# Optimization experiments

Measured on AMD Instinct MI355X. Metric: run time of the kernel, lower is better.

The kernel has to match this reference:

```python
import jax, jax.numpy as jnp
import numpy as np

N_NODES = 100000
N_EDGES = 3200000
N_FEAT = 16
N_GRAPHS = 1024


def setup_inputs() -> dict:
    key = jax.random.key(0)
    ks = jax.random.split(key, 12)
    x = jax.random.normal(ks[0], (N_NODES, N_FEAT), dtype=jnp.float32)
    edge_index = jax.random.randint(ks[1], (2, N_EDGES), 0, N_NODES, dtype=jnp.int32)
    batch = jnp.sort(jax.random.randint(ks[2], (N_NODES,), 0, N_GRAPHS, dtype=jnp.int32))
    def lin(k, fan_in, fan_out):
        s = 1.0 / np.sqrt(fan_in)
        return jax.random.uniform(k, (fan_in, fan_out), jnp.float32, -s, s)
    W1 = lin(ks[3], N_FEAT, 64); b1 = jnp.zeros((64,), jnp.float32)
    W2 = lin(ks[4], 64, 32);     b2 = jnp.zeros((32,), jnp.float32)
    fc1_W = lin(ks[5], 32, 16);  fc1_b = jnp.zeros((16,), jnp.float32)
    fc2_W = lin(ks[6], 16, 1);   fc2_b = jnp.zeros((1,), jnp.float32)
    return {"x": x, "edge_index": edge_index, "batch": batch,
            "W1": W1, "b1": b1, "W2": W2, "b2": b2,
            "fc1_W": fc1_W, "fc1_b": fc1_b, "fc2_W": fc2_W, "fc2_b": fc2_b}


def _gcn_conv(h, W, b, src, dst, norm, n_nodes):
    # h: [N, Fin] -> [N, Fout]; symmetric-normalized scatter-add (PyG GCNConv)
    h = h @ W
    msg = h[src] * norm[:, None]            # edge-wise gather + scale
    out = jax.ops.segment_sum(msg, dst, num_segments=n_nodes)
    return out + b


def reference(x, edge_index, batch, W1, b1, W2, b2, fc1_W, fc1_b, fc2_W, fc2_b):
    n_nodes = x.shape[0]
    # add self-loops
    loops = jnp.arange(n_nodes, dtype=edge_index.dtype)
    src = jnp.concatenate([edge_index[0], loops])
    dst = jnp.concatenate([edge_index[1], loops])
    deg = jax.ops.segment_sum(jnp.ones_like(dst, dtype=x.dtype), dst, num_segments=n_nodes)
    dinv = jnp.where(deg > 0, jax.lax.rsqrt(deg), 0.0)
    norm = dinv[src] * dinv[dst]

    h = jax.nn.relu(_gcn_conv(x, W1, b1, src, dst, norm, n_nodes))
    # dropout p=0.2 is identity at inference
    h = jax.nn.relu(_gcn_conv(h, W2, b2, src, dst, norm, n_nodes))

    # global mean pool over graphs
    sums = jax.ops.segment_sum(h, batch, num_segments=N_GRAPHS)
    cnts = jax.ops.segment_sum(jnp.ones((n_nodes,), h.dtype), batch, num_segments=N_GRAPHS)
    g = sums / jnp.maximum(cnts, 1.0)[:, None]

    g = jax.nn.relu(g @ fc1_W + fc1_b)
    # dropout p=0.5 is identity at inference
    out = g @ fc2_W + fc2_b
    return jax.nn.sigmoid(out)  # [N_GRAPHS, 1]
```

## Files before the change

### kernel.cpp

```cpp
#include <hip/hip_runtime.h>
#include <math.h>

#define NNODES  100000
#define NEDGES  3200000
#define NGRAPHS 1024
#define BNODES  196
#define NBUCK   ((NNODES + BNODES - 1) / BNODES)
#define SCAP    12288
#define CHUNK   4096
#define NCHUNKS ((NEDGES + CHUNK - 1) / CHUNK)

typedef int iv4 __attribute__((ext_vector_type(4)));
typedef float fv2 __attribute__((ext_vector_type(2)));

#if defined(__has_builtin)
#if __has_builtin(__builtin_amdgcn_cvt_pk_f32_fp8) && __has_builtin(__builtin_amdgcn_cvt_pk_fp8_f32)
#define HW_FP8 1
#endif
#endif

__device__ __forceinline__ unsigned bf16pair(float a, float b) {
    unsigned ua = __float_as_uint(a), ub = __float_as_uint(b);
    ua += 0x7fffu + ((ua >> 16) & 1u);
    ub += 0x7fffu + ((ub >> 16) & 1u);
    return (ua >> 16) | (ub & 0xffff0000u);
}
__device__ __forceinline__ float bflo(unsigned u) { return __uint_as_float(u << 16); }
__device__ __forceinline__ float bfhi(unsigned u) { return __uint_as_float(u & 0xffff0000u); }

__device__ __forceinline__ unsigned fp8_of(float v) {
    unsigned s = (__float_as_uint(v) >> 24) & 0x80u;
    float a = fminf(fabsf(v), 448.f);
    unsigned ub = __float_as_uint(a);
    unsigned lsb = (ub >> 20) & 1u;
    ub += 0x0007FFFFu + lsb;
    int em = (int)(ub >> 20) - (120 << 3);
    if (em < 1) return s;
    if (em > 0x7E) em = 0x7E;
    return s | (unsigned)em;
}
__device__ __forceinline__ float fp8_to_f(unsigned b) {
    unsigned em = b & 0x7Fu;
    unsigned s = (b & 0x80u) << 24;
    float f = __uint_as_float(s | ((em + 0x3C0u) << 20));
    return (em >= 8u) ? f : 0.f;
}
__device__ __forceinline__ void fp8x4_to_f(unsigned w, float& f0, float& f1, float& f2, float& f3) {
#ifdef HW_FP8
    fv2 lo = __builtin_amdgcn_cvt_pk_f32_fp8((int)w, false);
    fv2 hi = __builtin_amdgcn_cvt_pk_f32_fp8((int)w, true);
    f0 = lo.x; f1 = lo.y; f2 = hi.x; f3 = hi.y;
#else
    f0 = fp8_to_f(w & 0xFFu);
    f1 = fp8_to_f((w >> 8) & 0xFFu);
    f2 = fp8_to_f((w >> 16) & 0xFFu);
    f3 = fp8_to_f(w >> 24);
#endif
}
__device__ __forceinline__ unsigned fp8x4_pack(float a, float b, float c, float d) {
    a = fminf(fmaxf(a, -448.f), 448.f);
    b = fminf(fmaxf(b, -448.f), 448.f);
    c = fminf(fmaxf(c, -448.f), 448.f);
    d = fminf(fmaxf(d, -448.f), 448.f);
#ifdef HW_FP8
    int w = __builtin_amdgcn_cvt_pk_fp8_f32(a, b, 0, false);
    w = __builtin_amdgcn_cvt_pk_fp8_f32(c, d, w, true);
    return (unsigned)w;
#else
    return fp8_of(a) | (fp8_of(b) << 8) | (fp8_of(c) << 16) | (fp8_of(d) << 24);
#endif
}


__global__ void zero4_kernel(int4* p, int nvec) {
    int i = blockIdx.x * blockDim.x + threadIdx.x;
    if (i < nvec) p[i] = make_int4(0, 0, 0, 0);
}


__global__ void binA_kernel(const int* __restrict__ src, const int* __restrict__ dst,
                            int* __restrict__ bucketCur, int* __restrict__ stage) {
    __shared__ int lcnt[NBUCK + 1];
    __shared__ int boff[NBUCK + 1];
    __shared__ int gbase[NBUCK + 1];
    __shared__ int cur[NBUCK + 1];
    __shared__ int ssum[256];
    __shared__ int packed[CHUNK];
    __shared__ unsigned short bof[CHUNK];
    int tid = threadIdx.x;
    int beg = blockIdx.x * CHUNK;
    int end = beg + CHUNK; if (end > NEDGES) end = NEDGES;
    int cnt = end - beg;

    for (int i = tid; i <= NBUCK; i += 256) lcnt[i] = 0;
    __syncthreads();

    int ent[16];
    int bk[16];
#pragma unroll
    for (int it = 0; it < 4; ++it) {
        int e0 = beg + tid * 4 + it * 1024;
        if (e0 < end) {
            iv4 d4 = __builtin_nontemporal_load((const iv4*)(dst + e0));
            iv4 s4 = __builtin_nontemporal_load((const iv4*)(src + e0));
            int b;
            b = d4.x / BNODES; ent[it*4+0] = s4.x | ((d4.x - b*BNODES) << 17); bk[it*4+0] = b; atomicAdd(&lcnt[b], 1);
            b = d4.y / BNODES; ent[it*4+1] = s4.y | ((d4.y - b*BNODES) << 17); bk[it*4+1] = b; atomicAdd(&lcnt[b], 1);
            b = d4.z / BNODES; ent[it*4+2] = s4.z | ((d4.z - b*BNODES) << 17); bk[it*4+2] = b; atomicAdd(&lcnt[b], 1);
            b = d4.w / BNODES; ent[it*4+3] = s4.w | ((d4.w - b*BNODES) << 17); bk[it*4+3] = b; atomicAdd(&lcnt[b], 1);
        } else {
            bk[it*4+0] = -1; bk[it*4+1] = -1; bk[it*4+2] = -1; bk[it*4+3] = -1;
            ent[it*4+0] = 0; ent[it*4+1] = 0; ent[it*4+2] = 0; ent[it*4+3] = 0;
        }
    }
    __syncthreads();

    int b0 = 2 * tid, b1 = 2 * tid + 1;
    int c0 = lcnt[b0];
    int c1 = (b1 < NBUCK) ? lcnt[b1] : 0;
    int sum = c0 + c1;
    ssum[tid] = sum;
    __syncthreads();
    for (int o = 1; o < 256; o <<= 1) {
        int t = (tid >= o) ? ssum[tid - o] : 0;
        __syncthreads();
        ssum[tid] += t;
        __syncthreads();
    }
    int excl = ssum[tid] - sum;
    boff[b0] = excl; cur[b0] = excl;
    if (b1 < NBUCK) { boff[b1] = excl + c0; cur[b1] = excl + c0; }
    if (c0 > 0) gbase[b0] = atomicAdd(&bucketCur[b0], c0);
    if (b1 < NBUCK && c1 > 0) gbase[b1] = atomicAdd(&bucketCur[b1], c1);
    __syncthreads();

#pragma unroll
    for (int k = 0; k < 16; ++k) {
        int b = bk[k];
        if (b >= 0) {
            int p = atomicAdd(&cur[b], 1);
            packed[p] = ent[k];
            bof[p] = (unsigned short)b;
        }
    }
    __syncthreads();

    for (int i = tid; i < cnt; i += 256) {
        int b = bof[i];
        int addr = b * SCAP + gbase[b] + (i - boff[b]);
        stage[addr] = packed[i];
    }
}


__global__ void scanE_kernel(const int* __restrict__ bucketCur, int* __restrict__ ebase) {
    int lane = threadIdx.x;
    int run = 0;
    for (int base = 0; base < NBUCK; base += 64) {
        int idx = base + lane;
        int own = (idx < NBUCK) ? bucketCur[idx] : 0;
        int v = own;
        for (int o = 1; o < 64; o <<= 1) {
            int t = __shfl_up(v, o, 64);
            if (lane >= o) v += t;
        }
        if (idx < NBUCK) ebase[idx] = run + v - own;
        run += __shfl(v, 63, 64);
    }
}


__global__ void binB_kernel(const int* __restrict__ bucketCur, const int* __restrict__ ebase,
                            const int* __restrict__ stage, const float2* __restrict__ x,
                            int* __restrict__ entries, int* __restrict__ rowptr,
                            int* __restrict__ rowend, float* __restrict__ dinv,
                            unsigned* __restrict__ xs) {
    __shared__ int s[256];
    __shared__ int ncur[256];
    __shared__ float ndinv[256];
    int b = blockIdx.x;
    int cntE = bucketCur[b];
    int eb = ebase[b];
    int nlo = b * BNODES;
    int nn = NNODES - nlo; if (nn > BNODES) nn = BNODES;
    int sb = b * SCAP;
    int tid = threadIdx.x;

    s[tid] = 0;
    __syncthreads();
    for (int e = tid; e < cntE; e += 256) {
        unsigned w = (unsigned)stage[sb + e];
        atomicAdd(&s[w >> 17], 1);
    }
    __syncthreads();
    int v = s[tid];
    for (int o = 1; o < 256; o <<= 1) {
        int t = (tid >= o) ? s[tid - o] : 0;
        __syncthreads();
        s[tid] += t;
        __syncthreads();
    }
    int excl = s[tid] - v;
    ncur[tid] = excl;
    if (tid < nn) {
        rowptr[nlo + tid] = eb + excl;
        rowend[nlo + tid] = eb + excl + v;
        float di = rsqrtf((float)(v + 1));
        dinv[nlo + tid] = di;
        ndinv[tid] = di;
    }
    __syncthreads();
    for (int i = tid; i < nn * 8; i += 256) {
        int node = i >> 3, w = i & 7;
        float2 v2 = x[(size_t)(nlo + node) * 8 + w];
        float di = ndinv[node];
        xs[(nlo + node) * 8 + w] = bf16pair(v2.x * di, v2.y * di);
    }
    for (int e = tid; e < cntE; e += 256) {
        unsigned w = (unsigned)stage[sb + e];
        int dl = w >> 17;
        int slot = atomicAdd(&ncur[dl], 1);
        entries[eb + slot] = (int)(w & 0x1FFFFu);
    }
}


__global__ void gather1_mlp_kernel(const int* __restrict__ entries, const int* __restrict__ rowptr,
                                   const int* __restrict__ rowend, const float* __restrict__ dinv,
                                   const unsigned* __restrict__ xs,
                                   const float* __restrict__ W1, const float* __restrict__ b1,
                                   const float* __restrict__ W2, unsigned* __restrict__ hm2f) {
    __shared__ float w1s[16 * 64];
    __shared__ float w2s[64 * 32];
    __shared__ float bb1[64];
    __shared__ float axs[32][17];
    __shared__ float h1s[32][65];
    int tid = threadIdx.x;
    for (int i = tid; i < 16 * 64; i += 256) w1s[i] = W1[i];
    for (int i = tid; i < 64 * 32; i += 256) w2s[i] = W2[i];
    if (tid < 64) bb1[tid] = b1[tid];

    int t = blockIdx.x * 256 + tid;
    int n = t >> 3, lane = t & 7;
    int nl = tid >> 3;
    int beg = rowptr[n], end = rowend[n];
    unsigned self = xs[n * 8 + lane];
    float a0 = bflo(self), a1 = bfhi(self);
    for (int base = beg; base < end; base += 8) {
        int m = end - base; if (m > 8) m = 8;
        int s = (lane < m) ? __builtin_nontemporal_load(entries + base + lane) : 0;
        if (m == 8) {
#pragma unroll
            for (int j = 0; j < 8; ++j) {
                unsigned v = xs[__shfl(s, j, 8) * 8 + lane];
                a0 += bflo(v); a1 += bfhi(v);
            }
        } else {
            for (int j = 0; j < m; ++j) {
                unsigned v = xs[__shfl(s, j, 8) * 8 + lane];
                a0 += bflo(v); a1 += bfhi(v);
            }
        }
    }
    float di = dinv[n];
    axs[nl][lane * 2]     = a0 * di;
    axs[nl][lane * 2 + 1] = a1 * di;
    __syncthreads();

    {
        int j0 = lane * 8;
        float h[8];
#pragma unroll
        for (int jj = 0; jj < 8; ++jj) h[jj] = bb1[j0 + jj];
#pragma unroll
        for (int k = 0; k < 16; ++k) {
            float a = axs[nl][k];
            const float* wr = w1s + k * 64 + j0;
#pragma unroll
            for (int jj = 0; jj < 8; ++jj) h[jj] += a * wr[jj];
        }
#pragma unroll
        for (int jj = 0; jj < 8; ++jj) h1s[nl][j0 + jj] = fmaxf(h[jj], 0.f);
    }
    __syncthreads();

    {
        int j0 = lane * 4;
        float c[4] = {0.f, 0.f, 0.f, 0.f};
#pragma unroll
        for (int k = 0; k < 64; ++k) {
            float hv = h1s[nl][k];
            const float* wr = w2s + k * 32 + j0;
#pragma unroll
            for (int jj = 0; jj < 4; ++jj) c[jj] += hv * wr[jj];
        }
        float sc = di * 64.f;
        hm2f[n * 8 + lane] = fp8x4_pack(c[0] * sc, c[1] * sc, c[2] * sc, c[3] * sc);
    }
}


__global__ void gather2_pool_kernel(const int* __restrict__ entries, const int* __restrict__ rowptr,
                                    const int* __restrict__ rowend, const float* __restrict__ dinv,
                                    const unsigned* __restrict__ hm2f, const float4* __restrict__ b2,
                                    const int* __restrict__ batch,
                                    float* __restrict__ psum, float* __restrict__ pcnt) {
    __shared__ float lps[8][32];
    __shared__ float lpc[8];
    int tid = threadIdx.x;
    ((float*)lps)[tid] = 0.f;
    if (tid < 8) lpc[tid] = 0.f;

    int t = blockIdx.x * 256 + tid;
    int n = t >> 3, lane = t & 7;
    int g0 = batch[(blockIdx.x * 256) >> 3];
    int beg = rowptr[n], end = rowend[n];
    unsigned self = hm2f[n * 8 + lane];
    float a0, a1, a2, a3;
    fp8x4_to_f(self, a0, a1, a2, a3);
    __syncthreads();

    for (int base = beg; base < end; base += 8) {
        int m = end - base; if (m > 8) m = 8;
        int s = (lane < m) ? __builtin_nontemporal_load(entries + base + lane) : 0;
        if (m == 8) {
#pragma unroll
            for (int j = 0; j < 8; ++j) {
                unsigned v = hm2f[__shfl(s, j, 8) * 8 + lane];
                float f0, f1, f2, f3;
                fp8x4_to_f(v, f0, f1, f2, f3);
                a0 += f0; a1 += f1; a2 += f2; a3 += f3;
            }
        } else {
            for (int j = 0; j < m; ++j) {
                unsigned v = hm2f[__shfl(s, j, 8) * 8 + lane];
                float f0, f1, f2, f3;
                fp8x4_to_f(v, f0, f1, f2, f3);
                a0 += f0; a1 += f1; a2 += f2; a3 += f3;
            }
        }
    }
    float sc = dinv[n] * (1.0f / 64.f);
    float4 bb = b2[lane];
    float v0 = fmaxf(a0 * sc + bb.x, 0.f);
    float v1 = fmaxf(a1 * sc + bb.y, 0.f);
    float v2 = fmaxf(a2 * sc + bb.z, 0.f);
    float v3 = fmaxf(a3 * sc + bb.w, 0.f);
    int g = batch[n];
    int gr = g - g0;
    if (gr < 8) {
        float* pg = &lps[gr][lane * 4];
        atomicAdd(pg + 0, v0);
        atomicAdd(pg + 1, v1);
        atomicAdd(pg + 2, v2);
        atomicAdd(pg + 3, v3);
        if (lane == 0) atomicAdd(&lpc[gr], 1.0f);
    } else {
        float* pg = psum + g * 32 + lane * 4;
        atomicAdd(pg + 0, v0);
        atomicAdd(pg + 1, v1);
        atomicAdd(pg + 2, v2);
        atomicAdd(pg + 3, v3);
        if (lane == 0) atomicAdd(&pcnt[g], 1.0f);
    }
    __syncthreads();
    int grf = tid >> 5, f = tid & 31;
    float v = lps[grf][f];
    if (v != 0.f) atomicAdd(&psum[(g0 + grf) * 32 + f], v);
    if (f == 0) {
        float c = lpc[grf];
        if (c != 0.f) atomicAdd(&pcnt[g0 + grf], c);
    }
}


__global__ void head_kernel(const float* __restrict__ psum, const float* __restrict__ pcnt,
                            const float* __restrict__ fc1W, const float* __restrict__ fc1b,
                            const float* __restrict__ fc2W, const float* __restrict__ fc2b,
                            float* __restrict__ out) {
    int g = blockIdx.x * blockDim.x + threadIdx.x;
    if (g >= NGRAPHS) return;
    float inv = 1.0f / fmaxf(pcnt[g], 1.0f);
    float gv[32];
#pragma unroll
    for (int k = 0; k < 32; ++k) gv[k] = psum[g * 32 + k] * inv;
    float o = fc2b[0];
#pragma unroll
    for (int j = 0; j < 16; ++j) {
        float h = fc1b[j];
#pragma unroll
        for (int k = 0; k < 32; ++k) h += gv[k] * fc1W[k * 16 + j];
        h = fmaxf(h, 0.f);
        o += h * fc2W[j];
    }
    out[g] = 1.0f / (1.0f + expf(-o));
}


extern "C" void kernel_launch(void* const* d_in, const int* in_sizes, int n_in,
                              void* d_out, int out_size, void* d_ws, size_t ws_size,
                              hipStream_t stream) {
    const float* x    = (const float*)d_in[0];
    const int*   ei   = (const int*)d_in[1];
    const int*   batch= (const int*)d_in[2];
    const float* W1   = (const float*)d_in[3];
    const float* b1   = (const float*)d_in[4];
    const float* W2   = (const float*)d_in[5];
    const float* b2   = (const float*)d_in[6];
    const float* fc1W = (const float*)d_in[7];
    const float* fc1b = (const float*)d_in[8];
    const float* fc2W = (const float*)d_in[9];
    const float* fc2b = (const float*)d_in[10];
    float* out = (float*)d_out;

    const int* src = ei;
    const int* dst = ei + NEDGES;

    char* wsb = (char*)d_ws;
    int*      bucketCur = (int*)wsb;
    float*    psum      = (float*)(wsb + 2048);
    float*    pcnt      = (float*)(wsb + 133120);
    int*      ebase     = (int*)(wsb + 137216);
    float*    dinv      = (float*)(wsb + 139264);
    int*      rowptr    = (int*)(wsb + 539264);
    int*      rowend    = (int*)(wsb + 939264);
    int*      stage     = (int*)(wsb + 1339392);
    int*      entries   = (int*)(wsb + 26456064);
    unsigned* xs        = (unsigned*)(wsb + 39256064);
    unsigned* hm2f      = (unsigned*)(wsb + 42456064);

    const int B = 256;
    zero4_kernel<<<(8576 + B - 1) / B, B, 0, stream>>>((int4*)wsb, 8576);

    binA_kernel<<<NCHUNKS, B, 0, stream>>>(src, dst, bucketCur, stage);
    scanE_kernel<<<1, 64, 0, stream>>>(bucketCur, ebase);
    binB_kernel<<<NBUCK, B, 0, stream>>>(bucketCur, ebase, stage, (const float2*)x,
                                         entries, rowptr, rowend, dinv, xs);

    gather1_mlp_kernel<<<NNODES * 8 / B, B, 0, stream>>>(entries, rowptr, rowend, dinv, xs,
                                                         W1, b1, W2, hm2f);
    gather2_pool_kernel<<<NNODES * 8 / B, B, 0, stream>>>(entries, rowptr, rowend, dinv,
                                                          hm2f, (const float4*)b2,
                                                          batch, psum, pcnt);
    head_kernel<<<(NGRAPHS + B - 1) / B, B, 0, stream>>>(psum, pcnt, fc1W, fc1b, fc2W, fc2b, out);
}
```

Before: 258.3 us.

## Replace CSR build with per-bucket LDS atomic scatter aggregation

Drops the scan kernel and the second binning pass that built a CSR (rowptr/rowend/entries). Both gather kernels now run one block per destination bucket and stream that bucket's staged (src,dst) words, accumulating messages into a shared-memory accumulator with LDS float atomics. This removes the counting sort and the entries write/read traffic. In exchange it adds heavy LDS atomic contention, fewer blocks (one per 196-node bucket) and a serialized per-chunk MLP loop with extra barriers.

```diff
diff --git a/kernel.cpp b/kernel.cpp
--- a/kernel.cpp
+++ b/kernel.cpp
@@ -153,59 +153,27 @@
 }
 
 
-__global__ void scanE_kernel(const int* __restrict__ bucketCur, int* __restrict__ ebase) {
-    int lane = threadIdx.x;
-    int run = 0;
-    for (int base = 0; base < NBUCK; base += 64) {
-        int idx = base + lane;
-        int own = (idx < NBUCK) ? bucketCur[idx] : 0;
-        int v = own;
-        for (int o = 1; o < 64; o <<= 1) {
-            int t = __shfl_up(v, o, 64);
-            if (lane >= o) v += t;
-        }
-        if (idx < NBUCK) ebase[idx] = run + v - own;
-        run += __shfl(v, 63, 64);
-    }
-}
-
-
-__global__ void binB_kernel(const int* __restrict__ bucketCur, const int* __restrict__ ebase,
-                            const int* __restrict__ stage, const float2* __restrict__ x,
-                            int* __restrict__ entries, int* __restrict__ rowptr,
-                            int* __restrict__ rowend, float* __restrict__ dinv,
-                            unsigned* __restrict__ xs) {
-    __shared__ int s[256];
-    __shared__ int ncur[256];
-    __shared__ float ndinv[256];
+__global__ void binDeg_kernel(const int* __restrict__ bucketCur, const int* __restrict__ stage,
+                              const float2* __restrict__ x, float* __restrict__ dinv,
+                              unsigned* __restrict__ xs) {
+    __shared__ int hist[BNODES];
+    __shared__ float ndinv[BNODES];
     int b = blockIdx.x;
     int cntE = bucketCur[b];
-    int eb = ebase[b];
     int nlo = b * BNODES;
     int nn = NNODES - nlo; if (nn > BNODES) nn = BNODES;
     int sb = b * SCAP;
     int tid = threadIdx.x;
 
-    s[tid] = 0;
+    for (int i = tid; i < BNODES; i += 256) hist[i] = 0;
     __syncthreads();
     for (int e = tid; e < cntE; e += 256) {
         unsigned w = (unsigned)stage[sb + e];
-        atomicAdd(&s[w >> 17], 1);
-    }
-    __syncthreads();
-    int v = s[tid];
-    for (int o = 1; o < 256; o <<= 1) {
-        int t = (tid >= o) ? s[tid - o] : 0;
-        __syncthreads();
-        s[tid] += t;
-        __syncthreads();
-    }
-    int excl = s[tid] - v;
-    ncur[tid] = excl;
+        atomicAdd(&hist[w >> 17], 1);
+    }
+    __syncthreads();
     if (tid < nn) {
-        rowptr[nlo + tid] = eb + excl;
-        rowend[nlo + tid] = eb + excl + v;
-        float di = rsqrtf((float)(v + 1));
+        float di = rsqrtf((float)(hist[tid] + 1));
         dinv[nlo + tid] = di;
         ndinv[tid] = di;
     }
@@ -216,160 +184,164 @@
         float di = ndinv[node];
         xs[(nlo + node) * 8 + w] = bf16pair(v2.x * di, v2.y * di);
     }
-    for (int e = tid; e < cntE; e += 256) {
-        unsigned w = (unsigned)stage[sb + e];
-        int dl = w >> 17;
-        int slot = atomicAdd(&ncur[dl], 1);
-        entries[eb + slot] = (int)(w & 0x1FFFFu);
-    }
-}
-
-
-__global__ void gather1_mlp_kernel(const int* __restrict__ entries, const int* __restrict__ rowptr,
-                                   const int* __restrict__ rowend, const float* __restrict__ dinv,
-                                   const unsigned* __restrict__ xs,
+}
+
+
+__global__ void gather1_mlp_kernel(const int* __restrict__ bucketCur, const int* __restrict__ stage,
+                                   const float* __restrict__ dinv, const unsigned* __restrict__ xs,
                                    const float* __restrict__ W1, const float* __restrict__ b1,
                                    const float* __restrict__ W2, unsigned* __restrict__ hm2f) {
+    __shared__ float accum[BNODES][17];
     __shared__ float w1s[16 * 64];
     __shared__ float w2s[64 * 32];
     __shared__ float bb1[64];
-    __shared__ float axs[32][17];
     __shared__ float h1s[32][65];
     int tid = threadIdx.x;
+    int b = blockIdx.x;
+    int cntE = bucketCur[b];
+    int nlo = b * BNODES;
+    int nn = NNODES - nlo; if (nn > BNODES) nn = BNODES;
+    int sb = b * SCAP;
+    int lane = tid & 7;
+
+    for (int i = tid; i < BNODES * 17; i += 256) ((float*)accum)[i] = 0.f;
     for (int i = tid; i < 16 * 64; i += 256) w1s[i] = W1[i];
     for (int i = tid; i < 64 * 32; i += 256) w2s[i] = W2[i];
     if (tid < 64) bb1[tid] = b1[tid];
-
-    int t = blockIdx.x * 256 + tid;
-    int n = t >> 3, lane = t & 7;
+    __syncthreads();
+
+    for (int e = (tid >> 3); e < cntE; e += 32) {
+        unsigned w = (unsigned)stage[sb + e];
+        int s = (int)(w & 0x1FFFFu);
+        int dl = (int)(w >> 17);
+        unsigned v = xs[s * 8 + lane];
+        atomicAdd(&accum[dl][lane * 2],     bflo(v));
+        atomicAdd(&accum[dl][lane * 2 + 1], bfhi(v));
+    }
+    __syncthreads();
+
     int nl = tid >> 3;
-    int beg = rowptr[n], end = rowend[n];
-    unsigned self = xs[n * 8 + lane];
-    float a0 = bflo(self), a1 = bfhi(self);
-    for (int base = beg; base < end; base += 8) {
-        int m = end - base; if (m > 8) m = 8;
-        int s = (lane < m) ? __builtin_nontemporal_load(entries + base + lane) : 0;
-        if (m == 8) {
-#pragma unroll
-            for (int j = 0; j < 8; ++j) {
-                unsigned v = xs[__shfl(s, j, 8) * 8 + lane];
-                a0 += bflo(v); a1 += bfhi(v);
+    for (int c = 0; c < (BNODES + 31) / 32; ++c) {
+        int node = c * 32 + nl;
+        bool act = node < nn;
+        float di = 0.f;
+        if (act) {
+            di = dinv[nlo + node];
+            unsigned sf = xs[(nlo + node) * 8 + lane];
+            accum[node][lane * 2]     = (accum[node][lane * 2]     + bflo(sf)) * di;
+            accum[node][lane * 2 + 1] = (accum[node][lane * 2 + 1] + bfhi(sf)) * di;
+        }
+        if (act) {
+            int j0 = lane * 8;
+            float h[8];
+#pragma unroll
+            for (int jj = 0; jj < 8; ++jj) h[jj] = bb1[j0 + jj];
+#pragma unroll
+            for (int k = 0; k < 16; ++k) {
+                float a = accum[node][k];
+                const float* wr = w1s + k * 64 + j0;
+#pragma unroll
+                for (int jj = 0; jj < 8; ++jj) h[jj] += a * wr[jj];
             }
-        } else {
-            for (int j = 0; j < m; ++j) {
-                unsigned v = xs[__shfl(s, j, 8) * 8 + lane];
-                a0 += bflo(v); a1 += bfhi(v);
+#pragma unroll
+            for (int jj = 0; jj < 8; ++jj) h1s[nl][j0 + jj] = fmaxf(h[jj], 0.f);
+        }
+        __syncthreads();
+        if (act) {
+            int j0 = lane * 4;
+            float cc[4] = {0.f, 0.f, 0.f, 0.f};
+#pragma unroll
+            for (int k = 0; k < 64; ++k) {
+                float hv = h1s[nl][k];
+                const float* wr = w2s + k * 32 + j0;
+#pragma unroll
+                for (int jj = 0; jj < 4; ++jj) cc[jj] += hv * wr[jj];
             }
-        }
-    }
-    float di = dinv[n];
-    axs[nl][lane * 2]     = a0 * di;
-    axs[nl][lane * 2 + 1] = a1 * di;
-    __syncthreads();
-
-    {
-        int j0 = lane * 8;
-        float h[8];
-#pragma unroll
-        for (int jj = 0; jj < 8; ++jj) h[jj] = bb1[j0 + jj];
-#pragma unroll
-        for (int k = 0; k < 16; ++k) {
-            float a = axs[nl][k];
-            const float* wr = w1s + k * 64 + j0;
-#pragma unroll
-            for (int jj = 0; jj < 8; ++jj) h[jj] += a * wr[jj];
-        }
-#pragma unroll
-        for (int jj = 0; jj < 8; ++jj) h1s[nl][j0 + jj] = fmaxf(h[jj], 0.f);
-    }
-    __syncthreads();
-
-    {
-        int j0 = lane * 4;
-        float c[4] = {0.f, 0.f, 0.f, 0.f};
-#pragma unroll
-        for (int k = 0; k < 64; ++k) {
-            float hv = h1s[nl][k];
-            const float* wr = w2s + k * 32 + j0;
-#pragma unroll
-            for (int jj = 0; jj < 4; ++jj) c[jj] += hv * wr[jj];
-        }
-        float sc = di * 64.f;
-        hm2f[n * 8 + lane] = fp8x4_pack(c[0] * sc, c[1] * sc, c[2] * sc, c[3] * sc);
-    }
-}
-
-
-__global__ void gather2_pool_kernel(const int* __restrict__ entries, const int* __restrict__ rowptr,
-                                    const int* __restrict__ rowend, const float* __restrict__ dinv,
-                                    const unsigned* __restrict__ hm2f, const float4* __restrict__ b2,
-                                    const int* __restrict__ batch,
+            float sc = di * 64.f;
+            hm2f[(nlo + node) * 8 + lane] = fp8x4_pack(cc[0] * sc, cc[1] * sc, cc[2] * sc, cc[3] * sc);
+        }
+        __syncthreads();
+    }
+}
+
+
+__global__ void gather2_pool_kernel(const int* __restrict__ bucketCur, const int* __restrict__ stage,
+                                    const float* __restrict__ dinv, const unsigned* __restrict__ hm2f,
+                                    const float4* __restrict__ b2, const int* __restrict__ batch,
                                     float* __restrict__ psum, float* __restrict__ pcnt) {
+    __shared__ float accum[BNODES][33];
     __shared__ float lps[8][32];
     __shared__ float lpc[8];
     int tid = threadIdx.x;
+    int b = blockIdx.x;
+    int cntE = bucketCur[b];
+    int nlo = b * BNODES;
+    int nn = NNODES - nlo; if (nn > BNODES) nn = BNODES;
+    int sb = b * SCAP;
+    int lane = tid & 7;
+
+    for (int i = tid; i < BNODES * 33; i += 256) ((float*)accum)[i] = 0.f;
     ((float*)lps)[tid] = 0.f;
     if (tid < 8) lpc[tid] = 0.f;
-
-    int t = blockIdx.x * 256 + tid;
-    int n = t >> 3, lane = t & 7;
-    int g0 = batch[(blockIdx.x * 256) >> 3];
-    int beg = rowptr[n], end = rowend[n];
-    unsigned self = hm2f[n * 8 + lane];
-    float a0, a1, a2, a3;
-    fp8x4_to_f(self, a0, a1, a2, a3);
-    __syncthreads();
-
-    for (int base = beg; base < end; base += 8) {
-        int m = end - base; if (m > 8) m = 8;
-        int s = (lane < m) ? __builtin_nontemporal_load(entries + base + lane) : 0;
-        if (m == 8) {
-#pragma unroll
-            for (int j = 0; j < 8; ++j) {
-                unsigned v = hm2f[__shfl(s, j, 8) * 8 + lane];
-                float f0, f1, f2, f3;
-                fp8x4_to_f(v, f0, f1, f2, f3);
-                a0 += f0; a1 += f1; a2 += f2; a3 += f3;
+    int g0 = batch[nlo];
+    __syncthreads();
+
+    for (int e = (tid >> 3); e < cntE; e += 32) {
+        unsigned w = (unsigned)stage[sb + e];
+        int s = (int)(w & 0x1FFFFu);
+        int dl = (int)(w >> 17);
+        unsigned v = hm2f[s * 8 + lane];
+        float f0, f1, f2, f3;
+        fp8x4_to_f(v, f0, f1, f2, f3);
+        float* ar = &accum[dl][lane * 4];
+        atomicAdd(ar + 0, f0);
+        atomicAdd(ar + 1, f1);
+        atomicAdd(ar + 2, f2);
+        atomicAdd(ar + 3, f3);
+    }
+    __syncthreads();
+
+    int nl = tid >> 3;
+    float4 bb = b2[lane];
+    for (int c = 0; c < (BNODES + 31) / 32; ++c) {
+        int node = c * 32 + nl;
+        if (node < nn) {
+            int n = nlo + node;
+            unsigned sf = hm2f[n * 8 + lane];
+            float s0, s1, s2, s3;
+            fp8x4_to_f(sf, s0, s1, s2, s3);
+            float sc = dinv[n] * (1.0f / 64.f);
+            float* ar = &accum[node][lane * 4];
+            float v0 = fmaxf((ar[0] + s0) * sc + bb.x, 0.f);
+            float v1 = fmaxf((ar[1] + s1) * sc + bb.y, 0.f);
+            float v2 = fmaxf((ar[2] + s2) * sc + bb.z, 0.f);
+            float v3 = fmaxf((ar[3] + s3) * sc + bb.w, 0.f);
+            int g = batch[n];
+            int gr = g - g0;
+            if (gr < 8) {
+                float* pg = &lps[gr][lane * 4];
+                atomicAdd(pg + 0, v0);
+                atomicAdd(pg + 1, v1);
+                atomicAdd(pg + 2, v2);
+                atomicAdd(pg + 3, v3);
+                if (lane == 0) atomicAdd(&lpc[gr], 1.0f);
+            } else {
+                float* pg = psum + g * 32 + lane * 4;
+                atomicAdd(pg + 0, v0);
+                atomicAdd(pg + 1, v1);
+                atomicAdd(pg + 2, v2);
+                atomicAdd(pg + 3, v3);
+                if (lane == 0) atomicAdd(&pcnt[g], 1.0f);
             }
-        } else {
-            for (int j = 0; j < m; ++j) {
-                unsigned v = hm2f[__shfl(s, j, 8) * 8 + lane];
-                float f0, f1, f2, f3;
-                fp8x4_to_f(v, f0, f1, f2, f3);
-                a0 += f0; a1 += f1; a2 += f2; a3 += f3;
-            }
-        }
-    }
-    float sc = dinv[n] * (1.0f / 64.f);
-    float4 bb = b2[lane];
-    float v0 = fmaxf(a0 * sc + bb.x, 0.f);
-    float v1 = fmaxf(a1 * sc + bb.y, 0.f);
-    float v2 = fmaxf(a2 * sc + bb.z, 0.f);
-    float v3 = fmaxf(a3 * sc + bb.w, 0.f);
-    int g = batch[n];
-    int gr = g - g0;
-    if (gr < 8) {
-        float* pg = &lps[gr][lane * 4];
-        atomicAdd(pg + 0, v0);
-        atomicAdd(pg + 1, v1);
-        atomicAdd(pg + 2, v2);
-        atomicAdd(pg + 3, v3);
-        if (lane == 0) atomicAdd(&lpc[gr], 1.0f);
-    } else {
-        float* pg = psum + g * 32 + lane * 4;
-        atomicAdd(pg + 0, v0);
-        atomicAdd(pg + 1, v1);
-        atomicAdd(pg + 2, v2);
-        atomicAdd(pg + 3, v3);
-        if (lane == 0) atomicAdd(&pcnt[g], 1.0f);
+        }
     }
     __syncthreads();
     int grf = tid >> 5, f = tid & 31;
     float v = lps[grf][f];
     if (v != 0.f) atomicAdd(&psum[(g0 + grf) * 32 + f], v);
     if (f == 0) {
-        float c = lpc[grf];
-        if (c != 0.f) atomicAdd(&pcnt[g0 + grf], c);
+        float cc = lpc[grf];
+        if (cc != 0.f) atomicAdd(&pcnt[g0 + grf], cc);
     }
 }
 
@@ -420,27 +392,19 @@
     int*      bucketCur = (int*)wsb;
     float*    psum      = (float*)(wsb + 2048);
     float*    pcnt      = (float*)(wsb + 133120);
-    int*      ebase     = (int*)(wsb + 137216);
-    float*    dinv      = (float*)(wsb + 139264);
-    int*      rowptr    = (int*)(wsb + 539264);
-    int*      rowend    = (int*)(wsb + 939264);
-    int*      stage     = (int*)(wsb + 1339392);
-    int*      entries   = (int*)(wsb + 26456064);
-    unsigned* xs        = (unsigned*)(wsb + 39256064);
-    unsigned* hm2f      = (unsigned*)(wsb + 42456064);
+    float*    dinv      = (float*)(wsb + 137216);
+    int*      stage     = (int*)(wsb + 537600);
+    unsigned* xs        = (unsigned*)(wsb + 25654272);
+    unsigned* hm2f      = (unsigned*)(wsb + 28854272);
 
     const int B = 256;
     zero4_kernel<<<(8576 + B - 1) / B, B, 0, stream>>>((int4*)wsb, 8576);
 
     binA_kernel<<<NCHUNKS, B, 0, stream>>>(src, dst, bucketCur, stage);
-    scanE_kernel<<<1, 64, 0, stream>>>(bucketCur, ebase);
-    binB_kernel<<<NBUCK, B, 0, stream>>>(bucketCur, ebase, stage, (const float2*)x,
-                                         entries, rowptr, rowend, dinv, xs);
-
-    gather1_mlp_kernel<<<NNODES * 8 / B, B, 0, stream>>>(entries, rowptr, rowend, dinv, xs,
-                                                         W1, b1, W2, hm2f);
-    gather2_pool_kernel<<<NNODES * 8 / B, B, 0, stream>>>(entries, rowptr, rowend, dinv,
-                                                          hm2f, (const float4*)b2,
-                                                          batch, psum, pcnt);
+    binDeg_kernel<<<NBUCK, B, 0, stream>>>(bucketCur, stage, (const float2*)x, dinv, xs);
+
+    gather1_mlp_kernel<<<NBUCK, B, 0, stream>>>(bucketCur, stage, dinv, xs, W1, b1, W2, hm2f);
+    gather2_pool_kernel<<<NBUCK, B, 0, stream>>>(bucketCur, stage, dinv, hm2f,
+                                                 (const float4*)b2, batch, psum, pcnt);
     head_kernel<<<(NGRAPHS + B - 1) / B, B, 0, stream>>>(psum, pcnt, fc1W, fc1b, fc2W, fc2b, out);
 }
```

Result: slower. 975.3 us (+277.6%).
